# Kernel tuning notes

Measured on AMD Instinct MI355X. Metric: run time of the kernel, lower is better.

## Reference

```python
import jax, jax.numpy as jnp
import numpy as np

D_MODEL = 1024
NUM_HEADS = 16
HEAD_DIM = D_MODEL // NUM_HEADS
B, S = 2, 2048
EPS = 1e-8


def setup_inputs() -> dict:
    key = jax.random.key(0)
    ks = jax.random.split(key, 9)
    sc = 1.0 / np.sqrt(D_MODEL)
    return {
        "x": jax.random.normal(ks[0], (B, S, D_MODEL), jnp.float32),
        "wq": jax.random.normal(ks[1], (D_MODEL, D_MODEL), jnp.float32) * sc,
        "bq": jax.random.normal(ks[2], (D_MODEL,), jnp.float32) * 0.01,
        "wk": jax.random.normal(ks[3], (D_MODEL, D_MODEL), jnp.float32) * sc,
        "bk": jax.random.normal(ks[4], (D_MODEL,), jnp.float32) * 0.01,
        "wv": jax.random.normal(ks[5], (D_MODEL, D_MODEL), jnp.float32) * sc,
        "bv": jax.random.normal(ks[6], (D_MODEL,), jnp.float32) * 0.01,
        "wo": jax.random.normal(ks[7], (D_MODEL, D_MODEL), jnp.float32) * sc,
        "bo": jax.random.normal(ks[8], (D_MODEL,), jnp.float32) * 0.01,
    }


def reference(x, wq, bq, wk, bk, wv, bv, wo, bo):
    b, s, d = x.shape
    h, hd = NUM_HEADS, HEAD_DIM
    # projections (torch Linear: y = x W^T + b); reshape to [b, h, s, hd]
    def proj(w, bias):
        return (jnp.einsum('bsd,ed->bse', x, w) + bias).reshape(b, s, h, hd).transpose(0, 2, 1, 3)
    q = proj(wq, bq)
    k = proj(wk, bk)
    v = proj(wv, bv)
    scores = jnp.einsum('bhqd,bhkd->bhqk', q, k) / np.sqrt(hd)
    attn = jax.nn.softmax(scores, axis=-1)
    o = jnp.einsum('bhqk,bhkd->bhqd', attn, v)  # [b, h, s, hd]
    # per-position, per-head Gram-Schmidt exclusion: remove component of o[i]
    # along v[i] (the loop in the original is independent over positions)
    v_norm_sq = jnp.sum(v * v, axis=-1, keepdims=True)          # [b,h,s,1]
    align = jnp.sum(o * v, axis=-1, keepdims=True) / (v_norm_sq + EPS)
    o = o - align * v
    o = o.transpose(0, 2, 1, 3).reshape(b, s, d)
    return jnp.einsum('bsd,ed->bse', o, wo) + bo
```

## Files before the change

kernel.cpp:

```cpp
#include <hip/hip_runtime.h>
#include <stdint.h>

#define SEQ 2048
#define NTOK 4096
#define DM 1024

typedef __bf16 bf16x8 __attribute__((ext_vector_type(8)));
typedef __bf16 bf16x4 __attribute__((ext_vector_type(4)));
typedef float f32x4 __attribute__((ext_vector_type(4)));

__device__ __forceinline__ unsigned short f2bf(float f) {
  union { float f; unsigned u; } v; v.f = f;
  return (unsigned short)((v.u + 0x7fffu + ((v.u >> 16) & 1u)) >> 16);
}
__device__ __forceinline__ float bf2f(unsigned short s) {
  union { unsigned u; float f; } v; v.u = ((unsigned)s) << 16; return v.f;
}
__device__ __forceinline__ unsigned pkbf(float a, float b) {
  union { float f; unsigned u; } x, y; x.f = a; y.f = b;
  return __builtin_amdgcn_perm(y.u + 0x8000u, x.u + 0x8000u, 0x07060302u);
}

__device__ __forceinline__ void async16(const unsigned short* g, unsigned short* l) {
  __builtin_amdgcn_global_load_lds(
      (const __attribute__((address_space(1))) void*)g,
      (__attribute__((address_space(3))) void*)l, 16, 0, 0);
}

__global__ __launch_bounds__(256) void cast_all(
    const float* __restrict__ x, const float* __restrict__ wq,
    const float* __restrict__ wk, const float* __restrict__ wv,
    const float* __restrict__ wo, unsigned short* __restrict__ dst) {
  size_t i = ((size_t)blockIdx.x * 256 + threadIdx.x) * 4;
  const float* src; size_t off;
  if (i < (size_t)NTOK * DM) { src = x; off = i; }
  else {
    size_t j = i - (size_t)NTOK * DM;
    int s = (int)(j >> 20);
    src = (s == 0) ? wq : (s == 1) ? wk : (s == 2) ? wv : wo;
    off = j & 1048575u;
  }
  float4 f = *(const float4*)(src + off);
  ushort4 o;
  o.x = f2bf(f.x); o.y = f2bf(f.y); o.z = f2bf(f.z); o.w = f2bf(f.w);
  *(ushort4*)(dst + i) = o;
}


template<int MI>
__device__ __forceinline__ void stage_half(
    const unsigned short* __restrict__ A, const unsigned short* __restrict__ Bw,
    int m0, int n0, int kt, unsigned short* As, unsigned short* Bs) {
  const int tid = threadIdx.x;
  const int r = tid >> 2, c = tid & 3;
#pragma unroll
  for (int b = 0; b < MI / 2; ++b) {
    const int row = b * 64 + r;
    async16(A + (size_t)(m0 + row) * 1024 + kt + ((c ^ (row & 3)) << 3),
            As + row * 32 + c * 8);
  }
#pragma unroll
  for (int b = 0; b < 2; ++b) {
    const int row = b * 64 + r;
    async16(Bw + (size_t)(n0 + row) * 1024 + kt + ((c ^ (row & 3)) << 3),
            Bs + row * 32 + c * 8);
  }
}

__device__ __forceinline__ void pipe_bar0() {
  asm volatile("s_waitcnt vmcnt(0)\ns_barrier" ::: "memory");
}
template<int MI>
__device__ __forceinline__ void pipe_barN() {
  if constexpr (MI == 4) asm volatile("s_waitcnt vmcnt(4)\ns_barrier" ::: "memory");
  else                   asm volatile("s_waitcnt vmcnt(3)\ns_barrier" ::: "memory");
}

template<int MI>
__device__ __forceinline__ void gemm_pipe(
    const unsigned short* __restrict__ A, const unsigned short* __restrict__ Bw,
    int m0, int n0, f32x4 (&acc)[MI][4],
    unsigned short* AsBase, unsigned short* BsBase) {
  const int tid = threadIdx.x, lane = tid & 63, w = tid >> 6;
  const int wm16 = (w >> 1) * MI * 16, wn = (w & 1) * 64;
  const int quad = lane >> 4, l16 = lane & 15;
  constexpr int ASZ = MI * 32 * 32;
  constexpr int BSZ = 128 * 32;

  stage_half<MI>(A, Bw, m0, n0, 0,  AsBase,       BsBase);
  stage_half<MI>(A, Bw, m0, n0, 32, AsBase + ASZ, BsBase + BSZ);
  pipe_barN<MI>();

  int cur = 0;
  for (int p = 0; p < 32; ++p) {
    const unsigned short* As = AsBase + cur * ASZ;
    const unsigned short* Bs = BsBase + cur * BSZ;

    bf16x8 af[MI], bf[4];
    const int swz = ((quad ^ (l16 & 3)) << 3);
#pragma unroll
    for (int i = 0; i < MI; ++i)
      af[i] = *(const bf16x8*)(As + (wm16 + i * 16 + l16) * 32 + swz);
#pragma unroll
    for (int j = 0; j < 4; ++j)
      bf[j] = *(const bf16x8*)(Bs + (wn + j * 16 + l16) * 32 + swz);

    if (p + 2 < 32) {
      const int slot = (cur == 0) ? 2 : cur - 1;
      stage_half<MI>(A, Bw, m0, n0, (p + 2) * 32,
                     AsBase + slot * ASZ, BsBase + slot * BSZ);
    }

#pragma unroll
    for (int i = 0; i < MI; ++i)
#pragma unroll
      for (int j = 0; j < 4; ++j)
        acc[i][j] = __builtin_amdgcn_mfma_f32_16x16x32_bf16(af[i], bf[j], acc[i][j], 0, 0, 0);

    if (p < 30)       pipe_barN<MI>();
    else if (p == 30) pipe_bar0();
    cur = (cur == 2) ? 0 : cur + 1;
  }
}

__global__ __launch_bounds__(256, 3) void qkv_gemm(
    const unsigned short* __restrict__ xb,
    const unsigned short* __restrict__ wqb, const unsigned short* __restrict__ wkb,
    const unsigned short* __restrict__ wvb,
    const float* __restrict__ bq, const float* __restrict__ bk, const float* __restrict__ bv,
    unsigned short* __restrict__ Q, unsigned short* __restrict__ Kd,
    unsigned short* __restrict__ Vt) {
  __shared__ unsigned short As[3 * 128 * 32], Bs[3 * 128 * 32];
  const int gx = blockIdx.x;
  const int kind = gx >> 8;
  const int rr = gx & 255;
  const int tok = 4 * (rr & 7) + ((rr >> 3) & 3);
  const int oth = rr >> 5;
  const unsigned short* A; const unsigned short* Bw;
  int m0, n0;
  if (kind == 2) { A = wvb; Bw = xb; m0 = oth * 128; n0 = tok * 128; }
  else { A = xb; Bw = kind ? wkb : wqb; m0 = tok * 128; n0 = oth * 128; }

  f32x4 acc[4][4];
#pragma unroll
  for (int i = 0; i < 4; ++i)
#pragma unroll
    for (int j = 0; j < 4; ++j) { f32x4 z = {0.f, 0.f, 0.f, 0.f}; acc[i][j] = z; }
  gemm_pipe<4>(A, Bw, m0, n0, acc, As, Bs);

  const int lane = threadIdx.x & 63, w = threadIdx.x >> 6;
  const int quad = lane >> 4, l16 = lane & 15;
  const int wm = (w >> 1) * 64, wn = (w & 1) * 64;

  if (kind == 2) {
#pragma unroll
    for (int i = 0; i < 4; ++i)
#pragma unroll
      for (int j = 0; j < 4; ++j) {
        const int n = n0 + wn + j * 16 + l16;
        const int tb = n >> 11, s = n & 2047;
#pragma unroll
        for (int r = 0; r < 4; ++r) {
          const int m = m0 + wm + i * 16 + quad * 4 + r;
          const int h = m >> 6, d = m & 63;
          Vt[((size_t)(tb * 16 + h) * 64 + d) * SEQ + s] = f2bf(acc[i][j][r] + bv[m]);
        }
      }
  } else {
    const float* bias = (kind == 0) ? bq : bk;
    const float scale = (kind == 0) ? 0.180336880f : 1.0f;
#pragma unroll
    for (int i = 0; i < 4; ++i)
#pragma unroll
    for (int j = 0; j < 4; ++j) {
        const int col = n0 + wn + j * 16 + l16;
        const float bb = bias[col];
        const int h = col >> 6, d = col & 63;
#pragma unroll
        for (int r = 0; r < 4; ++r) {
          const int m = m0 + wm + i * 16 + quad * 4 + r;
          const int b = m >> 11, s = m & 2047;
          const int bh = b * 16 + h;
          const unsigned short val = f2bf((acc[i][j][r] + bb) * scale);
          if (kind == 0) Q[((size_t)bh * SEQ + s) * 64 + d] = val;
          else           Kd[((size_t)bh * SEQ + s) * 64 + d] = val;
        }
      }
  }
}

__global__ __launch_bounds__(128) void attn_kernel(
    const unsigned short* __restrict__ Q, const unsigned short* __restrict__ Kd,
    const unsigned short* __restrict__ Vt,
    unsigned short* __restrict__ O) {
  __shared__ unsigned short KV[4][4096];
  const int gx = blockIdx.x;
  const int xcd = gx & 7;
  const int idx = gx >> 3;
  const int bh  = xcd * 4 + (idx & 3);
  const int q0  = (idx >> 2) * 128;
  const int tid = threadIdx.x, lane = tid & 63, w = tid >> 6;
  const int quad = lane >> 4, l16 = lane & 15;
  const unsigned short* Qp = Q + (size_t)bh * SEQ * 64;
  const unsigned short* Kp = Kd + (size_t)bh * SEQ * 64;
  const unsigned short* Vp = Vt + (size_t)bh * 64 * SEQ;
  const int srow = tid >> 3;
  const int sc = ((tid & 7) ^ ((srow & 3) | ((srow & 8) >> 1))) << 3;

#pragma unroll
  for (int c = 0; c < 8; ++c)
    async16(Qp + (size_t)(q0 + c * 16 + srow) * 64 + sc,
            KV[c >> 2] + (c & 3) * 1024 + tid * 8);
  __syncthreads();

  const int gl = (l16 & 3) | ((l16 & 8) >> 1);
  const int sel = l16 & 7;
  const unsigned short* Qsrc = KV[w];
  bf16x8 bQ[4][2];
#pragma unroll
  for (int qq = 0; qq < 4; ++qq) {
    const int qrow = qq * 16 + l16;
#pragma unroll
    for (int hh = 0; hh < 2; ++hh)
      bQ[qq][hh] = *(const bf16x8*)(Qsrc + qrow * 64 + (((hh * 4 + quad) ^ gl) << 3));
  }
  __syncthreads();

  auto stageKV = [&](int kt, int nb) {
#pragma unroll
    for (int c = 0; c < 4; ++c)
      async16(Kp + (size_t)(kt + c * 16 + srow) * 64 + sc,
              KV[nb] + c * 1024 + tid * 8);
#pragma unroll
    for (int c = 0; c < 4; ++c)
      async16(Vp + (size_t)(c * 16 + srow) * SEQ + kt + sc,
              KV[2 + nb] + c * 1024 + tid * 8);
  };
  stageKV(0, 0);

  union { unsigned short u[8]; bf16x8 v; } one8;
#pragma unroll
  for (int t = 0; t < 8; ++t) one8.u[t] = 0x3F80;
  const bf16x8 aOnes = one8.v;

  f32x4 o_acc[4][4];
  f32x4 l_acc[4];
  const f32x4 zinit = {-12.f, -12.f, -12.f, -12.f};
#pragma unroll
  for (int qq = 0; qq < 4; ++qq) {
    f32x4 z = {0.f, 0.f, 0.f, 0.f};
    l_acc[qq] = z;
#pragma unroll
    for (int dt = 0; dt < 4; ++dt) o_acc[qq][dt] = z;
  }

  for (int it = 0; it < 32; ++it) {
    const int cur = it & 1;
    __syncthreads();
    if (it + 1 < 32) stageKV((it + 1) * 64, (it + 1) & 1);
    const unsigned short* Ks = KV[cur];
    const unsigned short* Vs = KV[2 + cur];

    __builtin_amdgcn_s_setprio(1);

    bf16x8 bP[4][2];
#pragma unroll
    for (int ee = 0; ee < 4; ++ee) {
      const int G = ee >> 1, e = ee & 1;
      const int R = G * 32 + ((l16 >> 2) << 3) + e * 4 + (l16 & 3);
      const unsigned short* arow = Ks + R * 64;
      bf16x8 a0 = *(const bf16x8*)(arow + ((quad ^ sel) << 3));
      bf16x8 a1 = *(const bf16x8*)(arow + (((4 + quad) ^ sel) << 3));
#pragma unroll
      for (int qq = 0; qq < 4; ++qq) {
        f32x4 z = __builtin_amdgcn_mfma_f32_16x16x32_bf16(a0, bQ[qq][0], zinit, 0, 0, 0);
        z = __builtin_amdgcn_mfma_f32_16x16x32_bf16(a1, bQ[qq][1], z, 0, 0, 0);
        const unsigned u0 = (unsigned)(int)__builtin_fmaf(z[0], 8388608.0f, 1065024977.0f);
        const unsigned u1 = (unsigned)(int)__builtin_fmaf(z[1], 8388608.0f, 1065024977.0f);
        const unsigned u2 = (unsigned)(int)__builtin_fmaf(z[2], 8388608.0f, 1065024977.0f);
        const unsigned u3 = (unsigned)(int)__builtin_fmaf(z[3], 8388608.0f, 1065024977.0f);
        union { unsigned d[4]; bf16x8 v; } pk;
        pk.v = bP[qq][G];
        pk.d[e * 2]     = __builtin_amdgcn_perm(u1, u0, 0x07060302u);
        pk.d[e * 2 + 1] = __builtin_amdgcn_perm(u3, u2, 0x07060302u);
        bP[qq][G] = pk.v;
      }
    }

#pragma unroll
    for (int qq = 0; qq < 4; ++qq)
#pragma unroll
      for (int G = 0; G < 2; ++G)
        l_acc[qq] = __builtin_amdgcn_mfma_f32_16x16x32_bf16(aOnes, bP[qq][G], l_acc[qq], 0, 0, 0);

#pragma unroll
    for (int dt = 0; dt < 4; ++dt) {
      const unsigned short* vbase = Vs + (dt * 16 + l16) * 64;
#pragma unroll
      for (int G = 0; G < 2; ++G) {
        bf16x8 aV = *(const bf16x8*)(vbase + (((G * 4 + quad) ^ gl) << 3));
#pragma unroll
        for (int qq = 0; qq < 4; ++qq)
          o_acc[qq][dt] = __builtin_amdgcn_mfma_f32_16x16x32_bf16(aV, bP[qq][G], o_acc[qq][dt], 0, 0, 0);
      }
    }

    __builtin_amdgcn_s_setprio(0);
  }

  const int b = bh >> 4, h = bh & 15;
#pragma unroll
  for (int qq = 0; qq < 4; ++qq) {
    const int qg = q0 + w * 64 + qq * 16 + l16;
    const float inv = 1.0f / l_acc[qq][0];
    const unsigned short* vp = Vp + qg;
    float ov = 0.f, v2 = 0.f;
#pragma unroll
    for (int dt = 0; dt < 4; ++dt)
#pragma unroll
      for (int r = 0; r < 4; ++r) {
        const int d = dt * 16 + quad * 4 + r;
        const float v = bf2f(vp[(size_t)d * SEQ]);
        ov += o_acc[qq][dt][r] * v;
        v2 += v * v;
      }
    ov *= inv;
    ov += __shfl_xor(ov, 16); ov += __shfl_xor(ov, 32);
    v2 += __shfl_xor(v2, 16); v2 += __shfl_xor(v2, 32);
    const float align = ov / (v2 + 1e-8f);
    unsigned short* dst = O + (size_t)(b * SEQ + qg) * DM + h * 64;
#pragma unroll
    for (int dt = 0; dt < 4; ++dt) {
      float a[4];
#pragma unroll
      for (int r = 0; r < 4; ++r) {
        const int d = dt * 16 + quad * 4 + r;
        const float v = bf2f(vp[(size_t)d * SEQ]);
        a[r] = __builtin_fmaf(o_acc[qq][dt][r], inv, -align * v);
      }
      uint2 pk2;
      pk2.x = pkbf(a[0], a[1]);
      pk2.y = pkbf(a[2], a[3]);
      *(uint2*)(dst + dt * 16 + quad * 4) = pk2;
    }
  }
}

__global__ __launch_bounds__(256, 3) void out_gemm(
    const unsigned short* __restrict__ Ob, const unsigned short* __restrict__ wob,
    const float* __restrict__ bo, float* __restrict__ out) {
  __shared__ unsigned short As[3 * 128 * 32], Bs[3 * 128 * 32];
  const int m0 = blockIdx.y * 128, n0 = blockIdx.x * 128;
  f32x4 acc[4][4];
#pragma unroll
  for (int i = 0; i < 4; ++i)
#pragma unroll
    for (int j = 0; j < 4; ++j) { f32x4 z = {0.f, 0.f, 0.f, 0.f}; acc[i][j] = z; }

  gemm_pipe<4>(Ob, wob, m0, n0, acc, As, Bs);

  const int lane = threadIdx.x & 63, w = threadIdx.x >> 6;
  const int quad = lane >> 4, l16 = lane & 15;
  const int wm = (w >> 1) * 64, wn = (w & 1) * 64;
#pragma unroll
  for (int i = 0; i < 4; ++i)
#pragma unroll
    for (int j = 0; j < 4; ++j) {
      const int col = n0 + wn + j * 16 + l16;
      const float bb = bo[col];
#pragma unroll
      for (int r = 0; r < 4; ++r) {
        const int m = m0 + wm + i * 16 + quad * 4 + r;
        out[(size_t)m * DM + col] = acc[i][j][r] + bb;
      }
    }
}

extern "C" void kernel_launch(void* const* d_in, const int* in_sizes, int n_in,
                              void* d_out, int out_size, void* d_ws, size_t ws_size,
                              hipStream_t stream) {
  const float* x  = (const float*)d_in[0];
  const float* wq = (const float*)d_in[1];
  const float* bq = (const float*)d_in[2];
  const float* wk = (const float*)d_in[3];
  const float* bk = (const float*)d_in[4];
  const float* wv = (const float*)d_in[5];
  const float* bv = (const float*)d_in[6];
  const float* wo = (const float*)d_in[7];
  const float* bo = (const float*)d_in[8];
  float* out = (float*)d_out;
  (void)in_sizes; (void)n_in; (void)out_size; (void)ws_size;

  unsigned short* ws  = (unsigned short*)d_ws;
  unsigned short* xb  = ws;
  unsigned short* wqb = xb + (size_t)NTOK * DM;
  unsigned short* wkb = wqb + (size_t)DM * DM;
  unsigned short* wvb = wkb + (size_t)DM * DM;
  unsigned short* wob = wvb + (size_t)DM * DM;
  unsigned short* Qb  = wob + (size_t)DM * DM;
  unsigned short* Kb  = Qb + (size_t)NTOK * DM;
  unsigned short* Vtb = Kb + (size_t)NTOK * DM;
  unsigned short* Ob  = Vtb + (size_t)NTOK * DM;

  cast_all<<<8192, 256, 0, stream>>>(x, wq, wk, wv, wo, ws);
  qkv_gemm<<<768, 256, 0, stream>>>(xb, wqb, wkb, wvb, bq, bk, bv, Qb, Kb, Vtb);
  attn_kernel<<<512, 128, 0, stream>>>(Qb, Kb, Vtb, Ob);
  out_gemm<<<dim3(8, 32), 256, 0, stream>>>(Ob, wob, bo, out);
}
```

Before: 201.3 us.

## Split attention KV range across two wave pairs and merge partials via LDS

The attention block grows from 2 to 4 waves. Each pair of waves processes half of the key/value sequence (split-K), so the loop runs 16 iterations instead of 32 over doubled LDS staging buffers. Partial output accumulators and row sums from the second pair are reduced through shared memory before the Gram-Schmidt epilogue. This aims to raise per-CU wave count and shorten the serial KV loop, at the cost of 64KB LDS per block, an extra reduction step, and half the waves idling in the epilogue. The softmax uses a fixed offset instead of a running max, which is what makes the plain sum of partials valid.

```diff
diff --git a/kernel.cpp b/kernel.cpp
--- a/kernel.cpp
+++ b/kernel.cpp
@@ -189,17 +189,21 @@
   }
 }
 
-__global__ __launch_bounds__(128) void attn_kernel(
+__global__ __launch_bounds__(256, 2) void attn_kernel(
     const unsigned short* __restrict__ Q, const unsigned short* __restrict__ Kd,
     const unsigned short* __restrict__ Vt,
     unsigned short* __restrict__ O) {
-  __shared__ unsigned short KV[4][4096];
+  __shared__ unsigned short SH[32768];
+#define KKB(g, b) (SH + ((g) * 2 + (b)) * 4096)
+#define VVB(g, b) (SH + 16384 + ((g) * 2 + (b)) * 4096)
   const int gx = blockIdx.x;
   const int xcd = gx & 7;
   const int idx = gx >> 3;
   const int bh  = xcd * 4 + (idx & 3);
   const int q0  = (idx >> 2) * 128;
   const int tid = threadIdx.x, lane = tid & 63, w = tid >> 6;
+  const int kp = w >> 1;
+  const int wq = w & 1;
   const int quad = lane >> 4, l16 = lane & 15;
   const unsigned short* Qp = Q + (size_t)bh * SEQ * 64;
   const unsigned short* Kp = Kd + (size_t)bh * SEQ * 64;
@@ -208,14 +212,14 @@
   const int sc = ((tid & 7) ^ ((srow & 3) | ((srow & 8) >> 1))) << 3;
 
 #pragma unroll
-  for (int c = 0; c < 8; ++c)
-    async16(Qp + (size_t)(q0 + c * 16 + srow) * 64 + sc,
-            KV[c >> 2] + (c & 3) * 1024 + tid * 8);
+  for (int c = 0; c < 4; ++c)
+    async16(Qp + (size_t)(q0 + c * 32 + srow) * 64 + sc,
+            KKB(0, c >> 1) + (c & 1) * 2048 + tid * 8);
   __syncthreads();
 
   const int gl = (l16 & 3) | ((l16 & 8) >> 1);
   const int sel = l16 & 7;
-  const unsigned short* Qsrc = KV[w];
+  const unsigned short* Qsrc = KKB(0, wq);
   bf16x8 bQ[4][2];
 #pragma unroll
   for (int qq = 0; qq < 4; ++qq) {
@@ -226,15 +230,15 @@
   }
   __syncthreads();
 
-  auto stageKV = [&](int kt, int nb) {
-#pragma unroll
-    for (int c = 0; c < 4; ++c)
-      async16(Kp + (size_t)(kt + c * 16 + srow) * 64 + sc,
-              KV[nb] + c * 1024 + tid * 8);
-#pragma unroll
-    for (int c = 0; c < 4; ++c)
-      async16(Vp + (size_t)(c * 16 + srow) * SEQ + kt + sc,
-              KV[2 + nb] + c * 1024 + tid * 8);
+  auto stageKV = [&](int it_, int nb) {
+#pragma unroll
+    for (int g = 0; g < 2; ++g) {
+      const int kt = g * 1024 + it_ * 64;
+      async16(Kp + (size_t)(kt + srow) * 64 + sc, KKB(g, nb) + tid * 8);
+      async16(Kp + (size_t)(kt + 32 + srow) * 64 + sc, KKB(g, nb) + 2048 + tid * 8);
+      async16(Vp + (size_t)srow * SEQ + kt + sc, VVB(g, nb) + tid * 8);
+      async16(Vp + (size_t)(32 + srow) * SEQ + kt + sc, VVB(g, nb) + 2048 + tid * 8);
+    }
   };
   stageKV(0, 0);
 
@@ -254,12 +258,12 @@
     for (int dt = 0; dt < 4; ++dt) o_acc[qq][dt] = z;
   }
 
-  for (int it = 0; it < 32; ++it) {
+  for (int it = 0; it < 16; ++it) {
     const int cur = it & 1;
     __syncthreads();
-    if (it + 1 < 32) stageKV((it + 1) * 64, (it + 1) & 1);
-    const unsigned short* Ks = KV[cur];
-    const unsigned short* Vs = KV[2 + cur];
+    if (it + 1 < 16) stageKV(it + 1, (it + 1) & 1);
+    const unsigned short* Ks = KKB(kp, cur);
+    const unsigned short* Vs = VVB(kp, cur);
 
     __builtin_amdgcn_s_setprio(1);
 
@@ -308,42 +312,67 @@
     __builtin_amdgcn_s_setprio(0);
   }
 
-  const int b = bh >> 4, h = bh & 15;
-#pragma unroll
-  for (int qq = 0; qq < 4; ++qq) {
-    const int qg = q0 + w * 64 + qq * 16 + l16;
-    const float inv = 1.0f / l_acc[qq][0];
-    const unsigned short* vp = Vp + qg;
-    float ov = 0.f, v2 = 0.f;
-#pragma unroll
-    for (int dt = 0; dt < 4; ++dt)
-#pragma unroll
-      for (int r = 0; r < 4; ++r) {
-        const int d = dt * 16 + quad * 4 + r;
-        const float v = bf2f(vp[(size_t)d * SEQ]);
-        ov += o_acc[qq][dt][r] * v;
-        v2 += v * v;
-      }
-    ov *= inv;
-    ov += __shfl_xor(ov, 16); ov += __shfl_xor(ov, 32);
-    v2 += __shfl_xor(v2, 16); v2 += __shfl_xor(v2, 32);
-    const float align = ov / (v2 + 1e-8f);
-    unsigned short* dst = O + (size_t)(b * SEQ + qg) * DM + h * 64;
-#pragma unroll
-    for (int dt = 0; dt < 4; ++dt) {
-      float a[4];
-#pragma unroll
-      for (int r = 0; r < 4; ++r) {
-        const int d = dt * 16 + quad * 4 + r;
-        const float v = bf2f(vp[(size_t)d * SEQ]);
-        a[r] = __builtin_fmaf(o_acc[qq][dt][r], inv, -align * v);
-      }
-      uint2 pk2;
-      pk2.x = pkbf(a[0], a[1]);
-      pk2.y = pkbf(a[2], a[3]);
-      *(uint2*)(dst + dt * 16 + quad * 4) = pk2;
-    }
-  }
+  __syncthreads();
+  float* xf = (float*)SH;
+  if (kp == 1) {
+    float* dst = xf + (size_t)(wq * 64 + lane) * 68;
+#pragma unroll
+    for (int qq = 0; qq < 4; ++qq)
+#pragma unroll
+      for (int dt = 0; dt < 4; ++dt)
+        *(f32x4*)(dst + qq * 16 + dt * 4) = o_acc[qq][dt];
+    f32x4 lv = {l_acc[0][0], l_acc[1][0], l_acc[2][0], l_acc[3][0]};
+    *(f32x4*)(dst + 64) = lv;
+  }
+  __syncthreads();
+  if (kp == 0) {
+    const float* src = xf + (size_t)(wq * 64 + lane) * 68;
+#pragma unroll
+    for (int qq = 0; qq < 4; ++qq)
+#pragma unroll
+      for (int dt = 0; dt < 4; ++dt)
+        o_acc[qq][dt] += *(const f32x4*)(src + qq * 16 + dt * 4);
+    const f32x4 lv = *(const f32x4*)(src + 64);
+
+    const int b = bh >> 4, h = bh & 15;
+#pragma unroll
+    for (int qq = 0; qq < 4; ++qq) {
+      const int qg = q0 + wq * 64 + qq * 16 + l16;
+      const float inv = 1.0f / (l_acc[qq][0] + lv[qq]);
+      const unsigned short* vp = Vp + qg;
+      float ov = 0.f, v2 = 0.f;
+#pragma unroll
+      for (int dt = 0; dt < 4; ++dt)
+#pragma unroll
+        for (int r = 0; r < 4; ++r) {
+          const int d = dt * 16 + quad * 4 + r;
+          const float v = bf2f(vp[(size_t)d * SEQ]);
+          ov += o_acc[qq][dt][r] * v;
+          v2 += v * v;
+        }
+      ov *= inv;
+      ov += __shfl_xor(ov, 16); ov += __shfl_xor(ov, 32);
+      v2 += __shfl_xor(v2, 16); v2 += __shfl_xor(v2, 32);
+      const float align = ov / (v2 + 1e-8f);
+      unsigned short* dst = O + (size_t)(b * SEQ + qg) * DM + h * 64;
+#pragma unroll
+      for (int dt = 0; dt < 4; ++dt) {
+        float a[4];
+#pragma unroll
+        for (int r = 0; r < 4; ++r) {
+          const int d = dt * 16 + quad * 4 + r;
+          const float v = bf2f(vp[(size_t)d * SEQ]);
+          a[r] = __builtin_fmaf(o_acc[qq][dt][r], inv, -align * v);
+        }
+        uint2 pk2;
+        pk2.x = pkbf(a[0], a[1]);
+        pk2.y = pkbf(a[2], a[3]);
+        *(uint2*)(dst + dt * 16 + quad * 4) = pk2;
+      }
+    }
+  }
+#undef KKB
+#undef VVB
 }
 
 __global__ __launch_bounds__(256, 3) void out_gemm(
@@ -404,6 +433,6 @@
 
   cast_all<<<8192, 256, 0, stream>>>(x, wq, wk, wv, wo, ws);
   qkv_gemm<<<768, 256, 0, stream>>>(xb, wqb, wkb, wvb, bq, bk, bv, Qb, Kb, Vtb);
-  attn_kernel<<<512, 128, 0, stream>>>(Qb, Kb, Vtb, Ob);
+  attn_kernel<<<512, 256, 0, stream>>>(Qb, Kb, Vtb, Ob);
   out_gemm<<<dim3(8, 32), 256, 0, stream>>>(Ob, wob, bo, out);
 }
```

Measured after the change: 177.9 us. 11.6% less time.
